# Kernel optimization log

Measured on AMD Instinct MI355X. Metric: run time of the kernel, lower is better.

The kernel has to match this reference:

```python
import jax, jax.numpy as jnp
import numpy as np

N = 1_000_000
D = 128
B = 10_000
NUM_STEP = 3
EPS = 1e-10


def setup_inputs() -> dict:
    key = jax.random.key(0)
    k1, k2, k3, k4, k5, k6 = jax.random.split(key, 6)
    x = jax.random.normal(k1, (N, D), dtype=jnp.float32)
    node2graph = jnp.sort(jax.random.randint(k2, (N,), 0, B)).astype(jnp.int64)
    s = 1.0 / np.sqrt(D)  # torch LSTM init scale
    w_ih = jax.random.uniform(k3, (4 * D, 2 * D), jnp.float32, -s, s)
    w_hh = jax.random.uniform(k4, (4 * D, D), jnp.float32, -s, s)
    b_ih = jax.random.uniform(k5, (4 * D,), jnp.float32, -s, s)
    b_hh = jax.random.uniform(k6, (4 * D,), jnp.float32, -s, s)
    return {"x": x, "w_ih": w_ih, "w_hh": w_hh, "b_ih": b_ih, "b_hh": b_hh,
            "node2graph": node2graph, "batch_size": B}


def _lstm_cell(inp, h, c, w_ih, w_hh, b_ih, b_hh):
    # PyTorch gate order: i, f, g, o
    gates = inp @ w_ih.T + b_ih + h @ w_hh.T + b_hh
    i, f, g, o = jnp.split(gates, 4, axis=-1)
    i = jax.nn.sigmoid(i)
    f = jax.nn.sigmoid(f)
    g = jnp.tanh(g)
    o = jax.nn.sigmoid(o)
    c = f * c + i * g
    h = o * jnp.tanh(c)
    return h, c


def reference(x, w_ih, w_hh, b_ih, b_hh, node2graph, batch_size):
    d = x.shape[-1]
    h = jnp.zeros((batch_size, d), x.dtype)
    c = jnp.zeros((batch_size, d), x.dtype)
    q_star = jnp.zeros((batch_size, 2 * d), x.dtype)
    for _ in range(NUM_STEP):
        h, c = _lstm_cell(q_star, h, c, w_ih, w_hh, b_ih, b_hh)
        query = h  # [B, d]
        # per-node logits: <query[g(n)], x[n]>
        prod = jnp.sum(query[node2graph] * x, axis=-1)  # [N]
        # segment softmax over graphs
        m = jax.ops.segment_max(prod, node2graph, num_segments=batch_size)
        e = jnp.exp(prod - m[node2graph])
        norm = jax.ops.segment_sum(e, node2graph, num_segments=batch_size)
        att = e / (norm[node2graph] + EPS)  # [N]
        out = jax.ops.segment_sum(att[:, None] * x, node2graph, num_segments=batch_size)  # [B, d]
        q_star = jnp.concatenate([query, out], axis=-1)
    return q_star
```

## Files before the change

kernel.cpp:

```cpp
#include <hip/hip_runtime.h>

#define D 128
#define EPS 1e-10f
#define TILE 16
#define TILE_H 32
#define WPB 4
#define NBLK 512
#define NBLK_H 512
#define THR 14.0f

typedef _Float16 hf2 __attribute__((ext_vector_type(2)));

__device__ __forceinline__ hf2 as_hf2(float v) { return __builtin_bit_cast(hf2, v); }
__device__ __forceinline__ float as_f32(hf2 v) { return __builtin_bit_cast(float, v); }

__device__ __forceinline__ float fdot2f(hf2 a, hf2 b, float c) {
#if __has_builtin(__builtin_amdgcn_fdot2)
    return __builtin_amdgcn_fdot2(a, b, c, false);
#else
    return (float)a.x * (float)b.x + (float)a.y * (float)b.y + c;
#endif
}

__device__ __forceinline__ void gload16(const void* g, void* l) {
    __builtin_amdgcn_global_load_lds(
        (const __attribute__((address_space(1))) void*)g,
        (__attribute__((address_space(3))) void*)l, 16, 0, 0);
}

__device__ __forceinline__ unsigned long long sload2(const int* rp, int idx) {
    unsigned long long r;
    int off = __builtin_amdgcn_readfirstlane(idx << 2);
    asm volatile("s_load_dwordx2 %0, %1, %2\n\ts_waitcnt lgkmcnt(0)"
                 : "=s"(r) : "s"(rp), "s"(off) : "memory");
    return r;
}

__device__ __forceinline__ void wait_vm(int nn) {
    switch (nn) {
    case 0:  asm volatile("s_waitcnt vmcnt(0)"  ::: "memory"); break;
    case 1:  asm volatile("s_waitcnt vmcnt(1)"  ::: "memory"); break;
    case 2:  asm volatile("s_waitcnt vmcnt(2)"  ::: "memory"); break;
    case 3:  asm volatile("s_waitcnt vmcnt(3)"  ::: "memory"); break;
    case 4:  asm volatile("s_waitcnt vmcnt(4)"  ::: "memory"); break;
    case 5:  asm volatile("s_waitcnt vmcnt(5)"  ::: "memory"); break;
    case 6:  asm volatile("s_waitcnt vmcnt(6)"  ::: "memory"); break;
    case 7:  asm volatile("s_waitcnt vmcnt(7)"  ::: "memory"); break;
    case 8:  asm volatile("s_waitcnt vmcnt(8)"  ::: "memory"); break;
    case 9:  asm volatile("s_waitcnt vmcnt(9)"  ::: "memory"); break;
    case 10: asm volatile("s_waitcnt vmcnt(10)" ::: "memory"); break;
    case 11: asm volatile("s_waitcnt vmcnt(11)" ::: "memory"); break;
    case 12: asm volatile("s_waitcnt vmcnt(12)" ::: "memory"); break;
    case 13: asm volatile("s_waitcnt vmcnt(13)" ::: "memory"); break;
    case 14: asm volatile("s_waitcnt vmcnt(14)" ::: "memory"); break;
    case 15: asm volatile("s_waitcnt vmcnt(15)" ::: "memory"); break;
    case 16: asm volatile("s_waitcnt vmcnt(16)" ::: "memory"); break;
    case 17: asm volatile("s_waitcnt vmcnt(17)" ::: "memory"); break;
    case 18: asm volatile("s_waitcnt vmcnt(18)" ::: "memory"); break;
    case 19: asm volatile("s_waitcnt vmcnt(19)" ::: "memory"); break;
    case 20: asm volatile("s_waitcnt vmcnt(20)" ::: "memory"); break;
    default: asm volatile("s_waitcnt vmcnt(0)"  ::: "memory"); break;
    }
}

__device__ __forceinline__ int dperm(int d) {
    return (d & 24) | ((d + 2 * (d >> 3)) & 7);
}
__device__ __forceinline__ int dperm_inv(int u) {
    int q = u >> 3;
    return (q << 3) | ((u - 2 * q) & 7);
}

__global__ void rowptr_kernel(const int* __restrict__ n2g, int N_, int B_,
                              int* __restrict__ row_ptr) {
    int b = blockIdx.x * 256 + threadIdx.x;
    if (b > B_) return;
    if (b == B_) { row_ptr[b] = N_; return; }
    int lo = 0, hi = N_;
    while (lo < hi) {
        int mid = (lo + hi) >> 1;
        if (n2g[mid] < b) lo = mid + 1; else hi = mid;
    }
    row_ptr[b] = lo;
}

__global__ void init_consts_kernel(const float* __restrict__ b_ih,
                                   const float* __restrict__ b_hh,
                                   float* __restrict__ b_sum,
                                   float* __restrict__ c1,
                                   float* __restrict__ h1) {
    int t = threadIdx.x;
    __shared__ float bs[512];
    float v = b_ih[t] + b_hh[t];
    b_sum[t] = v;
    bs[t] = v;
    __syncthreads();
    if (t < D) {
        float ig = 1.f / (1.f + __expf(-bs[t]));
        float gg = tanhf(bs[256 + t]);
        float c  = ig * gg;
        float og = 1.f / (1.f + __expf(-bs[384 + t]));
        c1[t] = c;
        h1[t] = og * tanhf(c);
    }
}

__global__ void init_w1_kernel(const float* __restrict__ w_ih,
                               const float* __restrict__ w_hh,
                               const float* __restrict__ b_sum,
                               const float* __restrict__ h1,
                               float* __restrict__ W1,
                               float* __restrict__ const2) {
    int j = blockIdx.x, k = threadIdx.x;
    float w = w_ih[j * 256 + k] + w_hh[j * 128 + k];
    W1[j * 128 + k] = w;
    __shared__ float red[128];
    red[k] = w * h1[k];
    __syncthreads();
    for (int s = 64; s > 0; s >>= 1) {
        if (k < s) red[k] += red[k + s];
        __syncthreads();
    }
    if (k == 0) const2[j] = b_sum[j] + red[0];
}

#define BM 64
#define BN 64
#define BK 32
__global__ __launch_bounds__(256) void lstm_gemm_kernel(
    const float* __restrict__ A1, const float* __restrict__ Wa, int wa_stride,
    const float* __restrict__ A2, const float* __restrict__ Wb, int wb_stride,
    const float* __restrict__ base, float* __restrict__ gates, int B_) {
    __shared__ float As[BM][BK / 2 + 1];
    __shared__ float Bs[BN][BK / 2 + 1];
    int b0 = blockIdx.y * BM;
    int j0 = blockIdx.x * BN;
    int tid = threadIdx.x;
    int tx = tid & 15, ty = tid >> 4;
    float acc[4][4] = {};
    int nphase = A2 ? 2 : 1;
    for (int phase = 0; phase < nphase; phase++) {
        const float* A = phase ? A2 : A1;
        const float* W = phase ? Wb : Wa;
        int ws = phase ? wb_stride : wa_stride;
        for (int k0 = 0; k0 < 128; k0 += BK) {
            __syncthreads();
            for (int i = tid; i < BM * (BK / 2); i += 256) {
                int r = i >> 4, cc = i & 15;
                int bb = b0 + r;
                float2 f2 = (bb < B_)
                    ? *(const float2*)&A[(size_t)bb * D + k0 + 2 * cc]
                    : make_float2(0.f, 0.f);
                hf2 h = {(_Float16)f2.x, (_Float16)f2.y};
                As[r][cc] = as_f32(h);
            }
            for (int i = tid; i < BN * (BK / 2); i += 256) {
                int r = i >> 4, cc = i & 15;
                float2 f2 = *(const float2*)&W[(size_t)(j0 + r) * ws + k0 + 2 * cc];
                hf2 h = {(_Float16)f2.x, (_Float16)f2.y};
                Bs[r][cc] = as_f32(h);
            }
            __syncthreads();
#pragma unroll
            for (int kk = 0; kk < BK / 2; kk++) {
                float av[4], bv[4];
#pragma unroll
                for (int i = 0; i < 4; i++) av[i] = As[ty * 4 + i][kk];
#pragma unroll
                for (int j = 0; j < 4; j++) bv[j] = Bs[tx * 4 + j][kk];
#pragma unroll
                for (int i = 0; i < 4; i++)
#pragma unroll
                    for (int j = 0; j < 4; j++)
                        acc[i][j] = fdot2f(as_hf2(av[i]), as_hf2(bv[j]),
                                           acc[i][j]);
            }
        }
    }
    for (int i = 0; i < 4; i++) {
        int bb = b0 + ty * 4 + i;
        if (bb >= B_) continue;
        for (int j = 0; j < 4; j++) {
            int jj = j0 + tx * 4 + j;
            gates[(size_t)bb * 512 + jj] = acc[i][j] + base[jj];
        }
    }
}

__global__ void lstm_elem_kernel(const float* __restrict__ gates,
                                 const float* __restrict__ c_prev, int c_bcast,
                                 float* __restrict__ c_out,
                                 float* __restrict__ h_out, int B_) {
    int t = blockIdx.x * 256 + threadIdx.x;
    if (t >= B_ * D) return;
    int b = t >> 7, d = t & (D - 1);
    const float* g = gates + (size_t)b * 512;
    float ig = 1.f / (1.f + __expf(-g[d]));
    float fg = 1.f / (1.f + __expf(-g[128 + d]));
    float gg = tanhf(g[256 + d]);
    float og = 1.f / (1.f + __expf(-g[384 + d]));
    float cp = c_bcast ? c_prev[d] : c_prev[t];
    float c = fg * cp + ig * gg;
    c_out[t] = c;
    h_out[t] = og * tanhf(c);
}

__global__ __launch_bounds__(256, 2) void attn_kernel(
    const float* __restrict__ x, const float* __restrict__ q_src, int q_bcast,
    const int* __restrict__ row_ptr, float* __restrict__ out,
    float* __restrict__ final_out, int B_, _Float16* __restrict__ xh) {

    __shared__ float xs[WPB][2][TILE * D];
    __shared__ float qs[WPB][2][256];
    __shared__ float wsh[WPB][TILE];

    const int tid  = threadIdx.x;
    const int wave = tid >> 6;
    const int lane = tid & 63;
    const int NW   = gridDim.x * WPB;

    const int p    = lane >> 5;
    const int sc   = lane & 31;
    const int n    = lane >> 2;
    const int qd   = lane & 3;
    const int qdb  = qd << 3;
    const int qd2  = qd << 1;
    const int dacc = dperm(sc);
    const int qsrc = dperm_inv(sc);

    float* xb[2] = {xs[wave][0], xs[wave][1]};
    float* qb[2] = {qs[wave][0], qs[wave][1]};
    float* wsw   = wsh[wave];

    auto issue_tile = [&](int t0, int e_, float* dst) {
#pragma unroll
        for (int j = 0; j < 8; j++) {
            int row = 2 * j + p;
            int rg  = t0 + row;
            rg = (rg < e_) ? rg : (e_ - 1);
            int u = (sc - row) & 31;
            int col = dperm_inv(u);
            gload16(x + ((size_t)rg * D + (col << 2)), dst + j * 256);
        }
    };
    auto issue_q = [&](int bq, float* dst) {
        const float* qp = q_bcast ? q_src : q_src + (size_t)bq * D;
        gload16(qp + (qsrc << 2), dst);
    };

    const int S = out ? 1 : 2;
    int b = blockIdx.x * WPB + wave;
    if (b >= B_) return;

    unsigned long long se0 = sload2(row_ptr, b);
    int s = (int)(se0 & 0xffffffffull), e = (int)(se0 >> 32);
    int cur = 0, qc = 0, ps = 0;
    issue_q(b, qb[0]);
    if (s < e) issue_tile(s, e, xb[0]);

    while (1) {
        float m = -1e30f, lsum = 0.f;
        float ax = 0.f, ay = 0.f, az = 0.f, aw = 0.f;
        int sn = 0, en = 0;
        int bn = b + NW;
        int have_next = (bn < B_);

        if (s < e) {
            for (int t0 = s; t0 < e; t0 += TILE) {
                int nt = e - t0; nt = (nt < TILE) ? nt : TILE;
                int just;
                if (t0 + TILE < e) {
                    issue_tile(t0 + TILE, e, xb[cur ^ 1]);
                    just = 8;
                } else if (have_next) {
                    unsigned long long se2 = sload2(row_ptr, bn);
                    sn = (int)(se2 & 0xffffffffull); en = (int)(se2 >> 32);
                    issue_q(bn, qb[qc ^ 1]);
                    just = 1;
                    if (sn < en) { issue_tile(sn, en, xb[cur ^ 1]); just = 9; }
                } else {
                    just = 0;
                }
                wait_vm(just + ps); ps = 0;

                const float4* xw4 = (const float4*)xb[cur];
                const float4* qw4 = (const float4*)qb[qc];

                if (xh) {
                    int row = n, qq = qd;
                    float dw[16];
#pragma unroll
                    for (int i = 0; i < 8; i++) {
                        int sl = ((qq * 8 + ((i + 2 * qq) & 7)) + row) & 31;
                        float4 f = xw4[(row << 5) + sl];
                        hf2 h0 = {(_Float16)f.x, (_Float16)f.y};
                        hf2 h1 = {(_Float16)f.z, (_Float16)f.w};
                        dw[2 * i]     = as_f32(h0);
                        dw[2 * i + 1] = as_f32(h1);
                    }
                    int rowg = t0 + row;
                    rowg = (rowg < e) ? rowg : (e - 1);
                    float4* xo = (float4*)((char*)xh +
                                 ((size_t)rowg * 256 + (qq << 6)));
                    xo[0] = make_float4(dw[0], dw[1], dw[2], dw[3]);
                    xo[1] = make_float4(dw[4], dw[5], dw[6], dw[7]);
                    xo[2] = make_float4(dw[8], dw[9], dw[10], dw[11]);
                    xo[3] = make_float4(dw[12], dw[13], dw[14], dw[15]);
                    ps += 4;
                }

                float pd0 = 0.f, pd1 = 0.f;
#pragma unroll
                for (int j = 0; j < 8; j += 2) {
                    int sl0 = ((qdb | ((j + qd2) & 7)) + n) & 31;
                    int sl1 = ((qdb | ((j + 1 + qd2) & 7)) + n) & 31;
                    float4 xv0 = xw4[(n << 5) + sl0];
                    float4 qv0 = qw4[qdb | ((j + qd2) & 7)];
                    float4 xv1 = xw4[(n << 5) + sl1];
                    float4 qv1 = qw4[qdb | ((j + 1 + qd2) & 7)];
                    pd0 += xv0.x * qv0.x + xv0.y * qv0.y + xv0.z * qv0.z + xv0.w * qv0.w;
                    pd1 += xv1.x * qv1.x + xv1.y * qv1.y + xv1.z * qv1.z + xv1.w * qv1.w;
                }
                float pd = pd0 + pd1;
                pd += __shfl_xor(pd, 1);
                pd += __shfl_xor(pd, 2);
                float prod = (n < nt) ? pd : -1e30f;

                if (!__all(prod <= m + THR)) {
                    float tmax = prod;
#pragma unroll
                    for (int mk = 4; mk <= 32; mk <<= 1)
                        tmax = fmaxf(tmax, __shfl_xor(tmax, mk));
                    float m_new = fmaxf(m, tmax);
                    float r = __expf(m - m_new);
                    lsum *= r;
                    ax *= r; ay *= r; az *= r; aw *= r;
                    m = m_new;
                }
                float w = __expf(prod - m);

                float tsum = w;
#pragma unroll
                for (int mk = 4; mk <= 32; mk <<= 1)
                    tsum += __shfl_xor(tsum, mk);
                lsum += tsum;

                if (qd == 0) wsw[n] = w;

#pragma unroll
                for (int i = 0; i < 8; i++) {
                    int row = 2 * i + p;
                    float wt = wsw[row];
                    float4 xv = xw4[(row << 5) + ((dacc + row) & 31)];
                    ax += wt * xv.x; ay += wt * xv.y;
                    az += wt * xv.z; aw += wt * xv.w;
                }
                cur ^= 1;
            }
        } else {
            int just = 0;
            if (have_next) {
                unsigned long long se2 = sload2(row_ptr, bn);
                sn = (int)(se2 & 0xffffffffull); en = (int)(se2 >> 32);
                issue_q(bn, qb[qc ^ 1]);
                just = 1;
                if (sn < en) { issue_tile(sn, en, xb[cur ^ 1]); just = 9; cur ^= 1; }
            }
            wait_vm(just + ps); ps = 0;
        }

        ax += __shfl_xor(ax, 32);
        ay += __shfl_xor(ay, 32);
        az += __shfl_xor(az, 32);
        aw += __shfl_xor(aw, 32);
        float inv = 1.f / (lsum + EPS);
        float4 o = {ax * inv, ay * inv, az * inv, aw * inv};
        if (p == 0) {
            if (out) {
                ((float4*)out)[(size_t)b * 32 + sc] = o;
            } else {
                const float4* q4r = (const float4*)qb[qc];
                float4 qv = q4r[dperm(sc)];
                float4* fo = (float4*)(final_out + (size_t)b * 256);
                fo[sc] = qv;
                fo[32 + sc] = o;
            }
        }
        ps += S;
        if (!have_next) break;
        b = bn; s = sn; e = en; qc ^= 1;
    }
}

__global__ __launch_bounds__(256, 2) void attn_h_kernel(
    const _Float16* __restrict__ xh, const float* __restrict__ q_src,
    const int* __restrict__ row_ptr, float* __restrict__ out,
    float* __restrict__ final_out, int B_) {

    __shared__ float xs[WPB][2][TILE_H * 64];
    __shared__ float qf[WPB][2][256];
    __shared__ float qh[WPB][64];
    __shared__ float wsh[WPB][TILE_H];

    const int tid  = threadIdx.x;
    const int wave = tid >> 6;
    const int lane = tid & 63;
    const int NW   = gridDim.x * WPB;

    const int n  = lane >> 1;
    const int h  = lane & 1;
    const int h8 = h << 3;
    const int g  = lane & 15;
    const int pp = lane >> 4;

    float* xb[2] = {xs[wave][0], xs[wave][1]};
    float* qb[2] = {qf[wave][0], qf[wave][1]};
    float* qhw   = qh[wave];
    float* wsw   = wsh[wave];

    auto issue_tile = [&](int t0, int e_, float* dst) {
#pragma unroll
        for (int j = 0; j < 8; j++) {
            int idx = (j << 6) + lane;
            int row = idx >> 4, s16 = idx & 15;
            int rg = t0 + row;
            rg = (rg < e_) ? rg : (e_ - 1);
            int gg = (s16 - row) & 15;
            gload16((const char*)xh + ((size_t)rg << 8) + (gg << 4),
                    dst + (j << 8));
        }
    };
    auto issue_q = [&](int bq, float* dst) {
        gload16(q_src + ((size_t)bq << 7) + ((lane & 31) << 2), dst);
    };

    const int S = out ? 2 : 4;
    int b = blockIdx.x * WPB + wave;
    if (b >= B_) return;

    unsigned long long se0 = sload2(row_ptr, b);
    int s = (int)(se0 & 0xffffffffull), e = (int)(se0 >> 32);
    int cur = 0, qc = 0, ps = 0;
    issue_q(b, qb[0]);
    if (s < e) issue_tile(s, e, xb[0]);

    while (1) {
        float m = -1e30f, lsum = 0.f;
        float a[8] = {0.f, 0.f, 0.f, 0.f, 0.f, 0.f, 0.f, 0.f};
        int sn = 0, en = 0;
        int bn = b + NW;
        int have_next = (bn < B_);

        if (s < e) {
            for (int t0 = s; t0 < e; t0 += TILE_H) {
                int nt = e - t0; nt = (nt < TILE_H) ? nt : TILE_H;
                int just;
                if (t0 + TILE_H < e) {
                    issue_tile(t0 + TILE_H, e, xb[cur ^ 1]);
                    just = 8;
                } else if (have_next) {
                    unsigned long long se2 = sload2(row_ptr, bn);
                    sn = (int)(se2 & 0xffffffffull); en = (int)(se2 >> 32);
                    issue_q(bn, qb[qc ^ 1]);
                    just = 1;
                    if (sn < en) { issue_tile(sn, en, xb[cur ^ 1]); just = 9; }
                } else {
                    just = 0;
                }
                wait_vm(just + ps); ps = 0;

                if (t0 == s) {
                    float2 f2 = ((const float2*)qb[qc])[lane];
                    hf2 hq = {(_Float16)f2.x, (_Float16)f2.y};
                    qhw[lane] = as_f32(hq);
                }

                const float4* xw4 = (const float4*)xb[cur];
                const float4* qh4 = (const float4*)qhw;

                float pd0 = 0.f, pd1 = 0.f;
#pragma unroll
                for (int j = 0; j < 8; j++) {
                    int gg = h8 + j;
                    float4 xv = xw4[(n << 4) + ((gg + n) & 15)];
                    float4 qv = qh4[gg];
                    pd0 = fdot2f(as_hf2(xv.x), as_hf2(qv.x), pd0);
                    pd1 = fdot2f(as_hf2(xv.y), as_hf2(qv.y), pd1);
                    pd0 = fdot2f(as_hf2(xv.z), as_hf2(qv.z), pd0);
                    pd1 = fdot2f(as_hf2(xv.w), as_hf2(qv.w), pd1);
                }
                float pd = pd0 + pd1;
                pd += __shfl_xor(pd, 1);
                float prod = (n < nt) ? pd : -1e30f;

                if (!__all(prod <= m + THR)) {
                    float tmax = prod;
#pragma unroll
                    for (int mk = 2; mk <= 32; mk <<= 1)
                        tmax = fmaxf(tmax, __shfl_xor(tmax, mk));
                    float m_new = fmaxf(m, tmax);
                    float r = __expf(m - m_new);
                    lsum *= r;
#pragma unroll
                    for (int k = 0; k < 8; k++) a[k] *= r;
                    m = m_new;
                }
                float w = __expf(prod - m);

                float tsum = w;
#pragma unroll
                for (int mk = 2; mk <= 32; mk <<= 1)
                    tsum += __shfl_xor(tsum, mk);
                lsum += tsum;

                if (h == 0) wsw[n] = w;

#pragma unroll
                for (int i = 0; i < 8; i++) {
                    int ro = (i << 2) + pp;
                    float wt = wsw[ro];
                    float4 xv = xw4[(ro << 4) + ((g + ro) & 15)];
                    hf2 h0 = as_hf2(xv.x), h1 = as_hf2(xv.y);
                    hf2 h2 = as_hf2(xv.z), h3 = as_hf2(xv.w);
                    a[0] += wt * (float)h0.x; a[1] += wt * (float)h0.y;
                    a[2] += wt * (float)h1.x; a[3] += wt * (float)h1.y;
                    a[4] += wt * (float)h2.x; a[5] += wt * (float)h2.y;
                    a[6] += wt * (float)h3.x; a[7] += wt * (float)h3.y;
                }
                cur ^= 1;
            }
        } else {
            int just = 0;
            if (have_next) {
                unsigned long long se2 = sload2(row_ptr, bn);
                sn = (int)(se2 & 0xffffffffull); en = (int)(se2 >> 32);
                issue_q(bn, qb[qc ^ 1]);
                just = 1;
                if (sn < en) { issue_tile(sn, en, xb[cur ^ 1]); just = 9; cur ^= 1; }
            }
            wait_vm(just + ps); ps = 0;
        }

#pragma unroll
        for (int k = 0; k < 8; k++) {
            a[k] += __shfl_xor(a[k], 16);
            a[k] += __shfl_xor(a[k], 32);
        }
        float inv = 1.f / (lsum + EPS);
        if (pp == 0) {
            float4 o0 = {a[0] * inv, a[1] * inv, a[2] * inv, a[3] * inv};
            float4 o1 = {a[4] * inv, a[5] * inv, a[6] * inv, a[7] * inv};
            if (out) {
                float4* op = (float4*)(out + (size_t)b * D + (g << 3));
                op[0] = o0; op[1] = o1;
            } else {
                const float4* q4r = (const float4*)qb[qc];
                float4 q0 = q4r[g * 2], q1 = q4r[g * 2 + 1];
                float4* fo = (float4*)(final_out + (size_t)b * 256 + (g << 3));
                fo[0] = q0; fo[1] = q1;
                float4* fo2 = (float4*)(final_out + (size_t)b * 256 + D + (g << 3));
                fo2[0] = o0; fo2[1] = o1;
            }
        }
        ps += S;
        if (!have_next) break;
        b = bn; s = sn; e = en; qc ^= 1;
    }
}

extern "C" void kernel_launch(void* const* d_in, const int* in_sizes, int n_in,
                              void* d_out, int out_size, void* d_ws,
                              size_t ws_size, hipStream_t stream) {
    const float* x    = (const float*)d_in[0];
    const float* w_ih = (const float*)d_in[1];
    const float* w_hh = (const float*)d_in[2];
    const float* b_ih = (const float*)d_in[3];
    const float* b_hh = (const float*)d_in[4];
    const int*   n2g  = (const int*)d_in[5];

    int N_ = in_sizes[0] / D;
    int B_ = out_size / (2 * D);

    char* wsb = (char*)d_ws;
    size_t off = 0;
    auto carve = [&](size_t bytes) {
        void* pp = wsb + off;
        off = (off + bytes + 255) & ~(size_t)255;
        return pp;
    };
    int*   row_ptr = (int*)carve((size_t)(B_ + 1) * 4);
    float* b_sum   = (float*)carve(512 * 4);
    float* c1      = (float*)carve(D * 4);
    float* h1      = (float*)carve(D * 4);
    float* const2  = (float*)carve(512 * 4);
    float* W1      = (float*)carve((size_t)512 * D * 4);
    float* hbuf    = (float*)carve((size_t)B_ * D * 4);
    float* cbuf    = (float*)carve((size_t)B_ * D * 4);
    float* outbuf  = (float*)carve((size_t)B_ * D * 4);
    float* gates   = (float*)carve((size_t)B_ * 512 * 4);
    _Float16* xh   = (_Float16*)carve((size_t)N_ * D * 2);
    bool use_half = (off <= ws_size);

    const float* W2 = w_ih + D;

    rowptr_kernel<<<(B_ + 1 + 255) / 256, 256, 0, stream>>>(n2g, N_, B_, row_ptr);
    init_consts_kernel<<<1, 512, 0, stream>>>(b_ih, b_hh, b_sum, c1, h1);
    init_w1_kernel<<<512, 128, 0, stream>>>(w_ih, w_hh, b_sum, h1, W1, const2);

    dim3 ggrid(512 / BN, (B_ + BM - 1) / BM);
    int  egrid = (B_ * D + 255) / 256;

    if (use_half) {
        attn_kernel<<<NBLK, 256, 0, stream>>>(x, h1, 1, row_ptr, outbuf,
                                              nullptr, B_, xh);
        lstm_gemm_kernel<<<ggrid, 256, 0, stream>>>(outbuf, W2, 256, nullptr,
                                                    nullptr, 0, const2, gates, B_);
        lstm_elem_kernel<<<egrid, 256, 0, stream>>>(gates, c1, 1, cbuf, hbuf, B_);
        attn_h_kernel<<<NBLK_H, 256, 0, stream>>>(xh, hbuf, row_ptr, outbuf,
                                                  nullptr, B_);
        lstm_gemm_kernel<<<ggrid, 256, 0, stream>>>(hbuf, W1, 128, outbuf, W2, 256,
                                                    b_sum, gates, B_);
        lstm_elem_kernel<<<egrid, 256, 0, stream>>>(gates, cbuf, 0, cbuf, hbuf, B_);
        attn_h_kernel<<<NBLK_H, 256, 0, stream>>>(xh, hbuf, row_ptr, nullptr,
                                                  (float*)d_out, B_);
    } else {
        attn_kernel<<<NBLK, 256, 0, stream>>>(x, h1, 1, row_ptr, outbuf,
                                              nullptr, B_, nullptr);
        lstm_gemm_kernel<<<ggrid, 256, 0, stream>>>(outbuf, W2, 256, nullptr,
                                                    nullptr, 0, const2, gates, B_);
        lstm_elem_kernel<<<egrid, 256, 0, stream>>>(gates, c1, 1, cbuf, hbuf, B_);
        attn_kernel<<<NBLK, 256, 0, stream>>>(x, hbuf, 0, row_ptr, outbuf,
                                              nullptr, B_, nullptr);
        lstm_gemm_kernel<<<ggrid, 256, 0, stream>>>(hbuf, W1, 128, outbuf, W2, 256,
                                                    b_sum, gates, B_);
        lstm_elem_kernel<<<egrid, 256, 0, stream>>>(gates, cbuf, 0, cbuf, hbuf, B_);
        attn_kernel<<<NBLK, 256, 0, stream>>>(x, hbuf, 0, row_ptr, nullptr,
                                              (float*)d_out, B_, nullptr);
    }
}
```

Before: 433.5 us.

## Merge setup kernels, store LSTM gates in fp16, move x→fp16 write into accumulate loop

Folds the row-pointer search, bias/constant init and W1 precompute into one setup kernel, with each block recomputing h1 locally so the separate launches and the dependency between them go away. LSTM gate pre-activations are now stored as fp16, halving that intermediate's memory traffic at some cost in precision. The fp16 conversion of x during the first attention pass moves from its own block of code into the weighted-accumulate loop, reusing the x values already loaded from LDS. The store pattern changes to narrower 8-byte writes, and the outstanding-store count used for the wait changes from 4 to 8 per tile.

```diff
diff --git a/kernel.cpp b/kernel.cpp
--- a/kernel.cpp
+++ b/kernel.cpp
@@ -71,57 +71,50 @@
     return (q << 3) | ((u - 2 * q) & 7);
 }
 
-__global__ void rowptr_kernel(const int* __restrict__ n2g, int N_, int B_,
-                              int* __restrict__ row_ptr) {
-    int b = blockIdx.x * 256 + threadIdx.x;
-    if (b > B_) return;
-    if (b == B_) { row_ptr[b] = N_; return; }
-    int lo = 0, hi = N_;
-    while (lo < hi) {
-        int mid = (lo + hi) >> 1;
-        if (n2g[mid] < b) lo = mid + 1; else hi = mid;
+__global__ __launch_bounds__(128) void setup_kernel(
+    const int* __restrict__ n2g, int N_, int B_, int* __restrict__ row_ptr,
+    const float* __restrict__ w_ih, const float* __restrict__ w_hh,
+    const float* __restrict__ b_ih, const float* __restrict__ b_hh,
+    float* __restrict__ W1, float* __restrict__ const2,
+    float* __restrict__ b_sum, float* __restrict__ c1,
+    float* __restrict__ h1) {
+    int blk = blockIdx.x;
+    if (blk < 512) {
+        int j = blk, k = threadIdx.x;
+        float w = w_ih[j * 256 + k] + w_hh[j * 128 + k];
+        W1[j * 128 + k] = w;
+        float bk = b_ih[k] + b_hh[k];
+        float bg = b_ih[256 + k] + b_hh[256 + k];
+        float bo = b_ih[384 + k] + b_hh[384 + k];
+        float ig = 1.f / (1.f + __expf(-bk));
+        float gg = tanhf(bg);
+        float c  = ig * gg;
+        float og = 1.f / (1.f + __expf(-bo));
+        float h1k = og * tanhf(c);
+        if (j == 0) { c1[k] = c; h1[k] = h1k; }
+        __shared__ float red[128];
+        red[k] = w * h1k;
+        __syncthreads();
+        for (int s = 64; s > 0; s >>= 1) {
+            if (k < s) red[k] += red[k + s];
+            __syncthreads();
+        }
+        if (k == 0) {
+            float bs = b_ih[j] + b_hh[j];
+            b_sum[j] = bs;
+            const2[j] = bs + red[0];
+        }
+    } else {
+        int b = (blk - 512) * 128 + threadIdx.x;
+        if (b > B_) return;
+        if (b == B_) { row_ptr[b] = N_; return; }
+        int lo = 0, hi = N_;
+        while (lo < hi) {
+            int mid = (lo + hi) >> 1;
+            if (n2g[mid] < b) lo = mid + 1; else hi = mid;
+        }
+        row_ptr[b] = lo;
     }
-    row_ptr[b] = lo;
-}
-
-__global__ void init_consts_kernel(const float* __restrict__ b_ih,
-                                   const float* __restrict__ b_hh,
-                                   float* __restrict__ b_sum,
-                                   float* __restrict__ c1,
-                                   float* __restrict__ h1) {
-    int t = threadIdx.x;
-    __shared__ float bs[512];
-    float v = b_ih[t] + b_hh[t];
-    b_sum[t] = v;
-    bs[t] = v;
-    __syncthreads();
-    if (t < D) {
-        float ig = 1.f / (1.f + __expf(-bs[t]));
-        float gg = tanhf(bs[256 + t]);
-        float c  = ig * gg;
-        float og = 1.f / (1.f + __expf(-bs[384 + t]));
-        c1[t] = c;
-        h1[t] = og * tanhf(c);
-    }
-}
-
-__global__ void init_w1_kernel(const float* __restrict__ w_ih,
-                               const float* __restrict__ w_hh,
-                               const float* __restrict__ b_sum,
-                               const float* __restrict__ h1,
-                               float* __restrict__ W1,
-                               float* __restrict__ const2) {
-    int j = blockIdx.x, k = threadIdx.x;
-    float w = w_ih[j * 256 + k] + w_hh[j * 128 + k];
-    W1[j * 128 + k] = w;
-    __shared__ float red[128];
-    red[k] = w * h1[k];
-    __syncthreads();
-    for (int s = 64; s > 0; s >>= 1) {
-        if (k < s) red[k] += red[k + s];
-        __syncthreads();
-    }
-    if (k == 0) const2[j] = b_sum[j] + red[0];
 }
 
 #define BM 64
@@ -130,7 +123,7 @@
 __global__ __launch_bounds__(256) void lstm_gemm_kernel(
     const float* __restrict__ A1, const float* __restrict__ Wa, int wa_stride,
     const float* __restrict__ A2, const float* __restrict__ Wb, int wb_stride,
-    const float* __restrict__ base, float* __restrict__ gates, int B_) {
+    const float* __restrict__ base, _Float16* __restrict__ gates, int B_) {
     __shared__ float As[BM][BK / 2 + 1];
     __shared__ float Bs[BN][BK / 2 + 1];
     int b0 = blockIdx.y * BM;
@@ -182,23 +175,23 @@
         if (bb >= B_) continue;
         for (int j = 0; j < 4; j++) {
             int jj = j0 + tx * 4 + j;
-            gates[(size_t)bb * 512 + jj] = acc[i][j] + base[jj];
+            gates[(size_t)bb * 512 + jj] = (_Float16)(acc[i][j] + base[jj]);
         }
     }
 }
 
-__global__ void lstm_elem_kernel(const float* __restrict__ gates,
+__global__ void lstm_elem_kernel(const _Float16* __restrict__ gates,
                                  const float* __restrict__ c_prev, int c_bcast,
                                  float* __restrict__ c_out,
                                  float* __restrict__ h_out, int B_) {
     int t = blockIdx.x * 256 + threadIdx.x;
     if (t >= B_ * D) return;
     int b = t >> 7, d = t & (D - 1);
-    const float* g = gates + (size_t)b * 512;
-    float ig = 1.f / (1.f + __expf(-g[d]));
-    float fg = 1.f / (1.f + __expf(-g[128 + d]));
-    float gg = tanhf(g[256 + d]);
-    float og = 1.f / (1.f + __expf(-g[384 + d]));
+    const _Float16* g = gates + (size_t)b * 512;
+    float ig = 1.f / (1.f + __expf(-(float)g[d]));
+    float fg = 1.f / (1.f + __expf(-(float)g[128 + d]));
+    float gg = tanhf((float)g[256 + d]);
+    float og = 1.f / (1.f + __expf(-(float)g[384 + d]));
     float cp = c_bcast ? c_prev[d] : c_prev[t];
     float c = fg * cp + ig * gg;
     c_out[t] = c;
@@ -286,29 +279,6 @@
                 const float4* xw4 = (const float4*)xb[cur];
                 const float4* qw4 = (const float4*)qb[qc];
 
-                if (xh) {
-                    int row = n, qq = qd;
-                    float dw[16];
-#pragma unroll
-                    for (int i = 0; i < 8; i++) {
-                        int sl = ((qq * 8 + ((i + 2 * qq) & 7)) + row) & 31;
-                        float4 f = xw4[(row << 5) + sl];
-                        hf2 h0 = {(_Float16)f.x, (_Float16)f.y};
-                        hf2 h1 = {(_Float16)f.z, (_Float16)f.w};
-                        dw[2 * i]     = as_f32(h0);
-                        dw[2 * i + 1] = as_f32(h1);
-                    }
-                    int rowg = t0 + row;
-                    rowg = (rowg < e) ? rowg : (e - 1);
-                    float4* xo = (float4*)((char*)xh +
-                                 ((size_t)rowg * 256 + (qq << 6)));
-                    xo[0] = make_float4(dw[0], dw[1], dw[2], dw[3]);
-                    xo[1] = make_float4(dw[4], dw[5], dw[6], dw[7]);
-                    xo[2] = make_float4(dw[8], dw[9], dw[10], dw[11]);
-                    xo[3] = make_float4(dw[12], dw[13], dw[14], dw[15]);
-                    ps += 4;
-                }
-
                 float pd0 = 0.f, pd1 = 0.f;
 #pragma unroll
                 for (int j = 0; j < 8; j += 2) {
@@ -352,9 +322,18 @@
                     int row = 2 * i + p;
                     float wt = wsw[row];
                     float4 xv = xw4[(row << 5) + ((dacc + row) & 31)];
+                    if (xh) {
+                        hf2 h0 = {(_Float16)xv.x, (_Float16)xv.y};
+                        hf2 h1 = {(_Float16)xv.z, (_Float16)xv.w};
+                        int rowg = t0 + row;
+                        rowg = (rowg < e) ? rowg : (e - 1);
+                        *(float2*)((char*)xh + ((size_t)rowg * 256 + (sc << 3)))
+                            = make_float2(as_f32(h0), as_f32(h1));
+                    }
                     ax += wt * xv.x; ay += wt * xv.y;
                     az += wt * xv.z; aw += wt * xv.w;
                 }
+                if (xh) ps += 8;
                 cur ^= 1;
             }
         } else {
@@ -588,24 +567,25 @@
         off = (off + bytes + 255) & ~(size_t)255;
         return pp;
     };
-    int*   row_ptr = (int*)carve((size_t)(B_ + 1) * 4);
-    float* b_sum   = (float*)carve(512 * 4);
-    float* c1      = (float*)carve(D * 4);
-    float* h1      = (float*)carve(D * 4);
-    float* const2  = (float*)carve(512 * 4);
-    float* W1      = (float*)carve((size_t)512 * D * 4);
-    float* hbuf    = (float*)carve((size_t)B_ * D * 4);
-    float* cbuf    = (float*)carve((size_t)B_ * D * 4);
-    float* outbuf  = (float*)carve((size_t)B_ * D * 4);
-    float* gates   = (float*)carve((size_t)B_ * 512 * 4);
-    _Float16* xh   = (_Float16*)carve((size_t)N_ * D * 2);
+    int*   row_ptr  = (int*)carve((size_t)(B_ + 1) * 4);
+    float* b_sum    = (float*)carve(512 * 4);
+    float* c1       = (float*)carve(D * 4);
+    float* h1       = (float*)carve(D * 4);
+    float* const2   = (float*)carve(512 * 4);
+    float* W1       = (float*)carve((size_t)512 * D * 4);
+    float* hbuf     = (float*)carve((size_t)B_ * D * 4);
+    float* cbuf     = (float*)carve((size_t)B_ * D * 4);
+    float* outbuf   = (float*)carve((size_t)B_ * D * 4);
+    _Float16* gates = (_Float16*)carve((size_t)B_ * 512 * 2);
+    _Float16* xh    = (_Float16*)carve((size_t)N_ * D * 2);
     bool use_half = (off <= ws_size);
 
     const float* W2 = w_ih + D;
 
-    rowptr_kernel<<<(B_ + 1 + 255) / 256, 256, 0, stream>>>(n2g, N_, B_, row_ptr);
-    init_consts_kernel<<<1, 512, 0, stream>>>(b_ih, b_hh, b_sum, c1, h1);
-    init_w1_kernel<<<512, 128, 0, stream>>>(w_ih, w_hh, b_sum, h1, W1, const2);
+    int sgrid = 512 + (B_ + 1 + 127) / 128;
+    setup_kernel<<<sgrid, 128, 0, stream>>>(n2g, N_, B_, row_ptr, w_ih, w_hh,
+                                            b_ih, b_hh, W1, const2, b_sum,
+                                            c1, h1);
 
     dim3 ggrid(512 / BN, (B_ + BM - 1) / BM);
     int  egrid = (B_ * D + 255) / 256;
```

New measurement: 407.7 us. -6.0%, faster.
